# Performance work log

Hardware: AMD Instinct MI355X
Metric: run time of the kernel (lower is better)

The kernel has to match this reference:

```python
import jax, jax.numpy as jnp
import numpy as np

B, H, T, K, V, S = 2, 8, 4096, 128, 128, 128
C = T // S


def setup_inputs() -> dict:
    key = jax.random.key(0)
    ks = jax.random.split(key, 5)
    return {
        "q": jax.random.normal(ks[0], (B, H, T, K), jnp.float32),
        "k": jax.random.normal(ks[1], (B, H, T, K), jnp.float32),
        "v": jax.random.normal(ks[2], (B, H, T, V), jnp.float32),
        "i": jax.random.normal(ks[3], (B, H, T), jnp.float32),
        "f": jax.random.normal(ks[4], (B, H, T), jnp.float32),
        "initial_C": jnp.zeros((B, H, K, V), jnp.float32),
        "initial_n": jnp.zeros((B, H, K), jnp.float32),
        "initial_m": jnp.zeros((B, H), jnp.float32),
    }


def _forward(q, k, v, ig, fg, C0, n0, m0):
    scale = 1.0 / np.sqrt(K)
    q = q.reshape(B, H, C, S, K) * scale
    k = k.reshape(B, H, C, S, K)
    v = v.reshape(B, H, C, S, V)
    i = ig.reshape(B, H, C, S)
    lf = jax.nn.log_sigmoid(fg).reshape(B, H, C, S)

    lfacc = jnp.cumsum(lf, axis=3)          # backward gates (intra-chunk cumsum)
    lflast = lfacc[..., -1]                  # (B,H,C) total log-forget per chunk
    # rev_cumsum_off: sum of log_fgates strictly after position t
    fwd_gates_unstab = i + (lflast[..., None] - lfacc)
    m_intra = jnp.max(fwd_gates_unstab, axis=3)          # (B,H,C)
    fgexp = jnp.exp(fwd_gates_unstab - m_intra[..., None])

    kv = jnp.einsum("bhctk,bhctd,bhct->bhckd", k, v, fgexp)
    ksum = jnp.einsum("bhctk,bhct->bhck", k, fgexp)

    # sequential inter-chunk recurrence over C chunks (stabilized)
    def step(carry, xs):
        c, n, m = carry
        kv_j, ks_j, lfl_j, mi_j = xs
        m_new = jnp.maximum(lfl_j + m, mi_j)
        e1 = jnp.exp(lfl_j + m - m_new)   # (B,H)
        e2 = jnp.exp(mi_j - m_new)
        out = (c, n, m)                    # state BEFORE this chunk
        c = c * e1[..., None, None] + kv_j * e2[..., None, None]
        n = n * e1[..., None] + ks_j * e2[..., None]
        return (c, n, m), out

    xs = (jnp.moveaxis(kv, 2, 0), jnp.moveaxis(ksum, 2, 0),
          jnp.moveaxis(lflast, 2, 0), jnp.moveaxis(m_intra, 2, 0))
    _, (c_prev, n_prev, m_prev) = jax.lax.scan(step, (C0, n0, m0), xs)
    c_prev = jnp.moveaxis(c_prev, 0, 2)   # (B,H,C,K,V)
    n_prev = jnp.moveaxis(n_prev, 0, 2)   # (B,H,C,K)
    m_prev = jnp.moveaxis(m_prev, 0, 2)   # (B,H,C)

    # intra-chunk causal forget matrix: G_unstab[s,t] = sum_{u=t+1..s} lf[u] + i[t]
    D = lfacc[..., :, None] - lfacc[..., None, :]        # (B,H,C,S,S)
    mask = jnp.tril(jnp.ones((S, S), bool))
    G_unstab = jnp.where(mask, D + i[:, :, :, None, :], -jnp.inf)
    G_stab = jnp.max(G_unstab, axis=-1)                   # (B,H,C,S)
    G_stab = jnp.maximum(G_stab, m_prev[..., None] + lfacc)
    G = jnp.exp(G_unstab - G_stab[..., None])             # -inf -> 0

    M = jnp.einsum("bhctk,bhcsk,bhcst->bhcst", k, q, G)
    inter_w = jnp.exp(lfacc + m_prev[..., None] - G_stab)  # (B,H,C,S)
    inter_n = jnp.einsum("bhcsk,bhcs,bhck->bhcs", q, inter_w, n_prev)
    M_norm = jnp.maximum(jnp.abs(M.sum(-1) + inter_n), jnp.exp(-G_stab))

    h = jnp.einsum("bhctv,bhcst,bhcs->bhcsv", v, M, 1.0 / M_norm)
    h = h + jnp.einsum("bhckv,bhcsk,bhcs->bhcsv", c_prev, q, inter_w / M_norm)
    return h.reshape(B, H, T, V)


def reference(q, k, v, i, f, initial_C, initial_n, initial_m):
    return _forward(q, k, v, i, f, initial_C, initial_n, initial_m)
```

## Files before the change

### kernel.cpp

```cpp
#include <hip/hip_runtime.h>
#include <hip/hip_fp16.h>
#include <math.h>

#define Bb 2
#define Hh 8
#define Tt 4096
#define Kk 128
#define Vv 128
#define Ss 128
#define Cc 32
#define BH (Bb*Hh)
#define SCALE 0.08838834764831845f

#define OFF_LFACC  0
#define OFF_LFLAST (OFF_LFACC + BH*Tt)
#define OFF_MINTRA (OFF_LFLAST + BH*Cc)
#define OFF_KSUM   (OFF_MINTRA + BH*Cc)
#define OFF_KVH    (OFF_KSUM + BH*Cc*Kk)
#define OFF_KIMG   (OFF_KVH + BH*Cc*Kk*Vv/2)
#define OFF_VIMG   (OFF_KIMG + BH*Tt*Kk/2)

typedef _Float16 f16x8 __attribute__((ext_vector_type(8)));
typedef _Float16 f16x4 __attribute__((ext_vector_type(4)));
typedef _Float16 f16x2 __attribute__((ext_vector_type(2)));
typedef float f32x4 __attribute__((ext_vector_type(4)));

union U2 { f16x2 h; unsigned u; };
union U8 { f16x8 v; unsigned u[4]; };

#define GLDS16(gp, lp) __builtin_amdgcn_global_load_lds( \
    (const __attribute__((address_space(1))) void*)(gp), \
    (__attribute__((address_space(3))) void*)(lp), 16, 0, 0)

__global__ __launch_bounds__(512, 4) void k_kvg(const float* __restrict__ ig,
                                                const float* __restrict__ fg,
                                                const float* __restrict__ kg,
                                                const float* __restrict__ vg,
                                                float* __restrict__ ws) {
    __shared__ _Float16 Kt[Ss * Ss];
    __shared__ _Float16 Vt[Ss * Ss];
    __shared__ float sfg[Ss];
    __shared__ float scomb[4];

    int blk = blockIdx.x;
    int bh = blk >> 5;
    int c  = blk & 31;
    int tid = threadIdx.x;
    int lane = tid & 63;
    int w = tid >> 6;
    int l15 = lane & 15;
    int g = lane >> 4;

    const float* kb = kg + ((size_t)bh * Tt + (size_t)c * Ss) * Kk;
    const float* vb = vg + ((size_t)bh * Tt + (size_t)c * Ss) * Vv;
    _Float16* kimgw = (_Float16*)(ws + OFF_KIMG) + (size_t)blk * Ss * Kk;
    _Float16* vimgw = (_Float16*)(ws + OFF_VIMG) + (size_t)blk * Ss * Kk;

    int c0a = (tid & 31) * 4;
    int t0a = (tid >> 5) * 4;
    const float* ksrcA = kb + (size_t)t0a * Kk + c0a;
    const float* vsrcA = vb + (size_t)t0a * Vv + c0a;
    float4 kA0 = *(const float4*)(ksrcA);
    float4 kA1 = *(const float4*)(ksrcA + Kk);
    float4 kA2 = *(const float4*)(ksrcA + 2 * Kk);
    float4 kA3 = *(const float4*)(ksrcA + 3 * Kk);
    float4 vA0 = *(const float4*)(vsrcA);
    float4 vA1 = *(const float4*)(vsrcA + Vv);
    float4 vA2 = *(const float4*)(vsrcA + 2 * Vv);
    float4 vA3 = *(const float4*)(vsrcA + 3 * Vv);
    int tau1 = tid + 512;
    int c0b = (tau1 & 31) * 4;
    int t0b = (tau1 >> 5) * 4;
    const float* ksrcB = kb + (size_t)t0b * Kk + c0b;
    const float* vsrcB = vb + (size_t)t0b * Vv + c0b;
    float4 kB0 = *(const float4*)(ksrcB);
    float4 kB1 = *(const float4*)(ksrcB + Kk);
    float4 kB2 = *(const float4*)(ksrcB + 2 * Kk);
    float4 kB3 = *(const float4*)(ksrcB + 3 * Kk);
    float4 vB0 = *(const float4*)(vsrcB);
    float4 vB1 = *(const float4*)(vsrcB + Vv);
    float4 vB2 = *(const float4*)(vsrcB + 2 * Vv);
    float4 vB3 = *(const float4*)(vsrcB + 3 * Vv);

    bool p0 = tid < Ss;
    int lane64 = tid & 63;
    int wv = (tid >> 6) & 1;
    int gidx = bh * Tt + c * Ss + tid;
    float lfacc = 0.f, fwd = 0.f;
    if (p0) {
        float x  = fg[gidx];
        lfacc = fminf(x, 0.f) - log1pf(__expf(-fabsf(x)));
        for (int off = 1; off < 64; off <<= 1) {
            float o = __shfl_up(lfacc, off);
            if (lane64 >= off) lfacc += o;
        }
        if (lane64 == 63) scomb[wv] = lfacc;
    }
    __syncthreads();
    if (p0) {
        float tot0 = scomb[0];
        if (wv == 1) lfacc += tot0;
        float lflast = tot0 + scomb[1];
        fwd = ig[gidx] + lflast - lfacc;
        float mx = fwd;
        for (int off = 32; off; off >>= 1) mx = fmaxf(mx, __shfl_xor(mx, off));
        if (lane64 == 0) scomb[2 + wv] = mx;
    }
    __syncthreads();
    if (p0) {
        float mi = fmaxf(scomb[2], scomb[3]);
        sfg[tid] = __expf(fwd - mi);
        ws[OFF_LFACC + gidx] = lfacc;
        if (tid == 0) {
            ws[OFF_LFLAST + blk] = scomb[0] + scomb[1];
            ws[OFF_MINTRA + blk] = mi;
        }
    }
    __syncthreads();

#pragma unroll
    for (int jr = 0; jr < 4; jr++) {
        float4 kr4 = (jr == 0 ? kA0 : jr == 1 ? kA1 : jr == 2 ? kA2 : kA3);
        int t = t0a + jr;
        int col = c0a ^ ((t & 15) << 3);
        f16x4 h = { (_Float16)kr4.x, (_Float16)kr4.y, (_Float16)kr4.z, (_Float16)kr4.w };
        *(f16x4*)&kimgw[(size_t)t * Kk + col] = h;
    }
#pragma unroll
    for (int jr = 0; jr < 4; jr++) {
        float4 kr4 = (jr == 0 ? kB0 : jr == 1 ? kB1 : jr == 2 ? kB2 : kB3);
        int t = t0b + jr;
        int col = c0b ^ ((t & 15) << 3);
        f16x4 h = { (_Float16)kr4.x, (_Float16)kr4.y, (_Float16)kr4.z, (_Float16)kr4.w };
        *(f16x4*)&kimgw[(size_t)t * Kk + col] = h;
    }

    {
        float g0 = sfg[t0a], g1 = sfg[t0a + 1], g2 = sfg[t0a + 2], g3 = sfg[t0a + 3];
#pragma unroll
        for (int jc = 0; jc < 4; jc++) {
            float ke0 = (jc == 0 ? kA0.x : jc == 1 ? kA0.y : jc == 2 ? kA0.z : kA0.w);
            float ke1 = (jc == 0 ? kA1.x : jc == 1 ? kA1.y : jc == 2 ? kA1.z : kA1.w);
            float ke2 = (jc == 0 ? kA2.x : jc == 1 ? kA2.y : jc == 2 ? kA2.z : kA2.w);
            float ke3 = (jc == 0 ? kA3.x : jc == 1 ? kA3.y : jc == 2 ? kA3.z : kA3.w);
            float ve0 = (jc == 0 ? vA0.x : jc == 1 ? vA0.y : jc == 2 ? vA0.z : vA0.w);
            float ve1 = (jc == 0 ? vA1.x : jc == 1 ? vA1.y : jc == 2 ? vA1.z : vA1.w);
            float ve2 = (jc == 0 ? vA2.x : jc == 1 ? vA2.y : jc == 2 ? vA2.z : vA2.w);
            float ve3 = (jc == 0 ? vA3.x : jc == 1 ? vA3.y : jc == 2 ? vA3.z : vA3.w);
            int row = c0a + jc;
            int col = t0a ^ ((row & 15) << 3);
            f16x4 kc = { (_Float16)(ke0 * g0), (_Float16)(ke1 * g1),
                         (_Float16)(ke2 * g2), (_Float16)(ke3 * g3) };
            f16x4 vc = { (_Float16)ve0, (_Float16)ve1, (_Float16)ve2, (_Float16)ve3 };
            *(f16x4*)&Kt[row * Ss + col] = kc;
            *(f16x4*)&Vt[row * Ss + col] = vc;
        }
    }
    {
        float g0 = sfg[t0b], g1 = sfg[t0b + 1], g2 = sfg[t0b + 2], g3 = sfg[t0b + 3];
#pragma unroll
        for (int jc = 0; jc < 4; jc++) {
            float ke0 = (jc == 0 ? kB0.x : jc == 1 ? kB0.y : jc == 2 ? kB0.z : kB0.w);
            float ke1 = (jc == 0 ? kB1.x : jc == 1 ? kB1.y : jc == 2 ? kB1.z : kB1.w);
            float ke2 = (jc == 0 ? kB2.x : jc == 1 ? kB2.y : jc == 2 ? kB2.z : kB2.w);
            float ke3 = (jc == 0 ? kB3.x : jc == 1 ? kB3.y : jc == 2 ? kB3.z : kB3.w);
            float ve0 = (jc == 0 ? vB0.x : jc == 1 ? vB0.y : jc == 2 ? vB0.z : vB0.w);
            float ve1 = (jc == 0 ? vB1.x : jc == 1 ? vB1.y : jc == 2 ? vB1.z : vB1.w);
            float ve2 = (jc == 0 ? vB2.x : jc == 1 ? vB2.y : jc == 2 ? vB2.z : vB2.w);
            float ve3 = (jc == 0 ? vB3.x : jc == 1 ? vB3.y : jc == 2 ? vB3.z : vB3.w);
            int row = c0b + jc;
            int col = t0b ^ ((row & 15) << 3);
            f16x4 kc = { (_Float16)(ke0 * g0), (_Float16)(ke1 * g1),
                         (_Float16)(ke2 * g2), (_Float16)(ke3 * g3) };
            f16x4 vc = { (_Float16)ve0, (_Float16)ve1, (_Float16)ve2, (_Float16)ve3 };
            *(f16x4*)&Kt[row * Ss + col] = kc;
            *(f16x4*)&Vt[row * Ss + col] = vc;
        }
    }
    __syncthreads();

#pragma unroll
    for (int p = 0; p < 4; p++)
        *(f16x8*)&vimgw[(size_t)(p * 512 + tid) * 8] =
            *(const f16x8*)&Vt[(p * 512 + tid) * 8];

    if (tid < Ss) {
        int sw = (tid & 15) << 3;
        float s = 0.f;
#pragma unroll
        for (int i = 0; i < 16; i++) {
            f16x8 ld = *(const f16x8*)&Kt[tid * Ss + ((8 * i) ^ sw)];
#pragma unroll
            for (int e = 0; e < 8; e++) s += (float)ld[e];
        }
        ws[OFF_KSUM + (size_t)blk * Kk + tid] = s;
    }

    const int band = w * 16;
    const int swt = l15 << 3;
    f16x8 af[4];
#pragma unroll
    for (int kk = 0; kk < 4; kk++)
        af[kk] = *(const f16x8*)&Vt[(band + l15) * Ss + ((kk * 32 + g * 8) ^ swt)];

    f32x4 acc[8];
#pragma unroll
    for (int kj = 0; kj < 8; kj++) acc[kj] = (f32x4){0.f, 0.f, 0.f, 0.f};

#pragma unroll
    for (int kj = 0; kj < 8; kj++) {
        int kr = kj * 16 + l15;
#pragma unroll
        for (int kk = 0; kk < 4; kk++) {
            f16x8 bv = *(const f16x8*)&Kt[kr * Ss + ((kk * 32 + g * 8) ^ swt)];
            acc[kj] = __builtin_amdgcn_mfma_f32_16x16x32_f16(af[kk], bv, acc[kj], 0, 0, 0);
        }
    }

    _Float16* dst = (_Float16*)(ws + OFF_KVH) + (size_t)blk * Kk * Vv;
#pragma unroll
    for (int kj = 0; kj < 8; kj++)
#pragma unroll
        for (int r = 0; r < 4; r++)
            dst[(size_t)(band + 4 * g + r) * Kk + kj * 16 + l15] = (_Float16)acc[kj][r];
}

__global__ __launch_bounds__(128) void k_scan_apply(const float* __restrict__ C0,
                                                    const float* __restrict__ n0,
                                                    const float* __restrict__ m0,
                                                    float* __restrict__ ws) {
    __shared__ float se1[Cc], se2[Cc];
    const int NC2 = BH * Kk * Vv / 2;
    int gid = blockIdx.x * 128 + threadIdx.x;
    bool main_r = gid < NC2;
    int bh = main_r ? (gid >> 13) : ((gid - NC2) >> 7);

    if (threadIdx.x < Cc) {
        int cc = threadIdx.x;
        float m   = m0[bh];
        float lfl = ws[OFF_LFLAST + bh * Cc + cc];
        float mi  = ws[OFF_MINTRA + bh * Cc + cc];
        float mn  = fmaxf(lfl + m, mi);
        se1[cc] = __expf(lfl + m - mn);
        se2[cc] = __expf(mi - mn);
    }
    __syncthreads();

    if (main_r) {
        int i  = gid & 8191;
        int v  = i >> 6;
        int k2 = (i & 63) << 1;
        float st0 = C0[(size_t)bh * Kk * Vv + (size_t)k2 * Vv + v];
        float st1 = C0[(size_t)bh * Kk * Vv + (size_t)(k2 + 1) * Vv + v];
        f16x2* base = (f16x2*)((_Float16*)(ws + OFF_KVH) +
                               (size_t)bh * Cc * Kk * Vv + (size_t)v * Kk + k2);
        const size_t stride = Kk * Vv / 2;
        f16x2 cur = base[0];
        f16x2 nxt = base[stride];
#pragma unroll
        for (int c = 0; c < Cc; c++) {
            f16x2 n2 = (c + 2 < Cc) ? base[(size_t)(c + 2) * stride]
                                    : (f16x2){(_Float16)0.f, (_Float16)0.f};
            f16x2 o = { (_Float16)st0, (_Float16)st1 };
            base[(size_t)c * stride] = o;
            float e1 = se1[c], e2 = se2[c];
            st0 = st0 * e1 + (float)cur[0] * e2;
            st1 = st1 * e1 + (float)cur[1] * e2;
            cur = nxt; nxt = n2;
        }
    } else if (gid < NC2 + BH * Kk) {
        int g2 = gid - NC2;
        float st = n0[g2];
        float* base = ws + OFF_KSUM + (size_t)bh * Cc * Kk + (g2 & (Kk - 1));
        float cur = base[0];
        float nxt = base[Kk];
#pragma unroll
        for (int c = 0; c < Cc; c++) {
            float n2 = (c + 2 < Cc) ? base[(size_t)(c + 2) * Kk] : 0.f;
            float kvv = cur;
            base[(size_t)c * Kk] = st;
            st = st * se1[c] + kvv * se2[c];
            cur = nxt; nxt = n2;
        }
    }
}

__global__ __launch_bounds__(512, 4) void k_out_mfma(const float* __restrict__ qg,
                                                     const float* __restrict__ ig,
                                                     const float* __restrict__ m0,
                                                     float* __restrict__ ws,
                                                     float* __restrict__ out) {
    __shared__ _Float16 XbK[Ss * Kk];
    __shared__ _Float16 XbV[Ss * Kk];
    __shared__ float sbt[Ss], sas[Ss], siw[Ss], slfa[Ss], snp[Ss];
    __shared__ float scomb[2];

    int blk = blockIdx.x;
    int bh = blk >> 5;
    int c  = blk & 31;
    int tid = threadIdx.x;
    int lane = tid & 63;
    int w = tid >> 6;
    int l15 = lane & 15;
    int g = lane >> 4;
    const int S0 = w * 16;
    const int swt = l15 << 3;

    const size_t rowbase = (size_t)bh * Tt + (size_t)c * Ss;
    const float* qp = qg + rowbase * Kk;
    const float* nprev = ws + OFF_KSUM + (size_t)blk * Kk;
    const _Float16* cprevT = (const _Float16*)(ws + OFF_KVH) + (size_t)blk * Kk * Vv;
    const _Float16* kimg = (const _Float16*)(ws + OFF_KIMG) + (size_t)blk * Ss * Kk;
    const _Float16* vimg = (const _Float16*)(ws + OFF_VIMG) + (size_t)blk * Ss * Kk;
    const float m_prev = m0[bh];

#pragma unroll
    for (int p = 0; p < 4; p++) {
        int unit = p * 512 + w * 64;
        GLDS16(kimg + (size_t)(unit + lane) * 8, &XbK[unit * 8]);
        GLDS16(vimg + (size_t)(unit + lane) * 8, &XbV[unit * 8]);
    }

    f16x8 qf[4];
#pragma unroll
    for (int kk = 0; kk < 4; kk++) {
        const float* p = qp + (size_t)(S0 + l15) * Kk + kk * 32 + g * 8;
        float4 a = *(const float4*)p;
        float4 b = *(const float4*)(p + 4);
        f16x8 r;
        r[0]=(_Float16)a.x; r[1]=(_Float16)a.y; r[2]=(_Float16)a.z; r[3]=(_Float16)a.w;
        r[4]=(_Float16)b.x; r[5]=(_Float16)b.y; r[6]=(_Float16)b.z; r[7]=(_Float16)b.w;
        qf[kk] = r;
    }

    bool p0 = tid < Ss;
    int lane64 = tid & 63;
    int wv = (tid >> 6) & 1;
    float pm = 0.f;
    if (p0) {
        float lfa = ws[OFF_LFACC + bh * Tt + c * Ss + tid];
        float bt = ig[bh * Tt + c * Ss + tid] - lfa;
        sbt[tid] = bt;
        slfa[tid] = lfa;
        snp[tid] = nprev[tid];
        pm = bt;
        for (int off = 1; off < 64; off <<= 1) {
            float o = __shfl_up(pm, off);
            if (lane64 >= off) pm = fmaxf(pm, o);
        }
        if (lane64 == 63) scomb[wv] = pm;
    }
    __syncthreads();

    if (p0) {
        if (wv == 1) pm = fmaxf(pm, scomb[0]);
        float mx = fmaxf(pm, m_prev);
        sas[tid] = -mx;
        siw[tid] = SCALE * __expf(m_prev - mx);
    }
    float dotq = 0.f;
#pragma unroll
    for (int kk = 0; kk < 4; kk++)
#pragma unroll
        for (int e = 0; e < 8; e++)
            dotq += (float)qf[kk][e] * snp[kk * 32 + g * 8 + e];
    dotq += __shfl_xor(dotq, 16);
    dotq += __shfl_xor(dotq, 32);
    __syncthreads();

    const float as_s = sas[S0 + l15];
    const float iw_s = siw[S0 + l15];
    const float lfa_s = slfa[S0 + l15];

    unsigned plo[8] = {0,0,0,0,0,0,0,0};
    unsigned phi[8] = {0,0,0,0,0,0,0,0};
    float rs = 0.f;
#pragma unroll
    for (int tj = 0; tj < 8; tj++) {
        if (tj <= w) {
            int trow = tj * 16 + l15;
            f16x8 bfr[4];
#pragma unroll
            for (int kk = 0; kk < 4; kk++)
                bfr[kk] = *(const f16x8*)&XbK[trow * Kk + ((kk * 32 + g * 8) ^ swt)];
            f32x4 acc = {0.f, 0.f, 0.f, 0.f};
#pragma unroll
            for (int kk = 0; kk < 4; kk++)
                acc = __builtin_amdgcn_mfma_f32_16x16x32_f16(bfr[kk], qf[kk], acc, 0, 0, 0);
            float vals[4];
#pragma unroll
            for (int r = 0; r < 4; r++) {
                int t = tj * 16 + 4 * g + r;
                float btv = sbt[t];
                float val = acc[r] * SCALE * __expf(as_s + btv);
                if (tj == w && (4 * g + r) > l15) val = 0.f;
                rs += val;
                vals[r] = val;
            }
            U2 lo, hi;
            lo.h = (f16x2){ (_Float16)vals[0], (_Float16)vals[1] };
            hi.h = (f16x2){ (_Float16)vals[2], (_Float16)vals[3] };
            plo[tj] = lo.u;
            phi[tj] = hi.u;
        }
    }
    rs += __shfl_xor(rs, 16);
    rs += __shfl_xor(rs, 32);
    float engs = __expf(as_s - lfa_s);
    float rnv_s = 1.0f / fmaxf(fabsf(rs + dotq * iw_s), engs);

    f16x8 pb[4];
    const int kmax = w >> 1;
    {
        int a2 = (g & 1) * 2;
        int sA = a2 * 16 + l15;
        int sB = sA + 16;
        bool hi2 = (g >> 1) != 0;
#pragma unroll
        for (int kkt = 0; kkt < 4; kkt++) {
            if (kkt <= kmax) {
                unsigned xA0 = __shfl((int)plo[2*kkt],   sA);
                unsigned xA1 = __shfl((int)phi[2*kkt],   sA);
                unsigned xB0 = __shfl((int)plo[2*kkt],   sB);
                unsigned xB1 = __shfl((int)phi[2*kkt],   sB);
                unsigned yA0 = __shfl((int)plo[2*kkt+1], sA);
                unsigned yA1 = __shfl((int)phi[2*kkt+1], sA);
                unsigned yB0 = __shfl((int)plo[2*kkt+1], sB);
                unsigned yB1 = __shfl((int)phi[2*kkt+1], sB);
                U8 t;
                t.u[0] = hi2 ? yA0 : xA0;
                t.u[1] = hi2 ? yA1 : xA1;
                t.u[2] = hi2 ? yB0 : xB0;
                t.u[3] = hi2 ? yB1 : xB1;
                pb[kkt] = t.v;
            }
        }
    }

#pragma unroll
    for (int half = 0; half < 2; half++) {
        f32x4 h4[4];
#pragma unroll
        for (int j = 0; j < 4; j++) h4[j] = (f32x4){0.f, 0.f, 0.f, 0.f};

#pragma unroll
        for (int kkt = 0; kkt < 4; kkt++) {
            if (kkt <= kmax) {
#pragma unroll
                for (int j = 0; j < 4; j++) {
                    int vr = (half * 4 + j) * 16 + l15;
                    f16x8 av = *(const f16x8*)&XbV[vr * Ss + ((kkt * 32 + g * 8) ^ swt)];
                    h4[j] = __builtin_amdgcn_mfma_f32_16x16x32_f16(av, pb[kkt], h4[j], 0, 0, 0);
                }
            }
        }
#pragma unroll
        for (int j = 0; j < 4; j++) {
            int vr = (half * 4 + j) * 16 + l15;
            f32x4 tmp = {0.f, 0.f, 0.f, 0.f};
            const _Float16* cpr = cprevT + (size_t)vr * Kk + g * 8;
#pragma unroll
            for (int kk = 0; kk < 4; kk++) {
                f16x8 bcf = *(const f16x8*)(cpr + kk * 32);
                tmp = __builtin_amdgcn_mfma_f32_16x16x32_f16(bcf, qf[kk], tmp, 0, 0, 0);
            }
            float4 o;
            o.x = (h4[j][0] + tmp[0] * iw_s) * rnv_s;
            o.y = (h4[j][1] + tmp[1] * iw_s) * rnv_s;
            o.z = (h4[j][2] + tmp[2] * iw_s) * rnv_s;
            o.w = (h4[j][3] + tmp[3] * iw_s) * rnv_s;
            *(float4*)&out[(rowbase + S0 + l15) * Vv + (half * 4 + j) * 16 + 4 * g] = o;
        }
    }
}

extern "C" void kernel_launch(void* const* d_in, const int* in_sizes, int n_in,
                              void* d_out, int out_size, void* d_ws, size_t ws_size,
                              hipStream_t stream) {
    (void)in_sizes; (void)n_in; (void)out_size; (void)ws_size;
    const float* q  = (const float*)d_in[0];
    const float* k  = (const float*)d_in[1];
    const float* v  = (const float*)d_in[2];
    const float* ig = (const float*)d_in[3];
    const float* fg = (const float*)d_in[4];
    const float* C0 = (const float*)d_in[5];
    const float* n0 = (const float*)d_in[6];
    const float* m0 = (const float*)d_in[7];
    float* out = (float*)d_out;
    float* ws  = (float*)d_ws;

    k_kvg<<<BH * Cc, 512, 0, stream>>>(ig, fg, k, v, ws);
    k_scan_apply<<<(BH * Kk * Vv / 2 + BH * Kk) / 128, 128, 0, stream>>>(C0, n0, m0, ws);
    k_out_mfma<<<BH * Cc, 512, 0, stream>>>(q, ig, m0, ws, out);
}
```

Before: 60.67 us.

## Stage swizzled C_prev tile into LDS asynchronously and reorder K-image writes

The output kernel used to read the per-chunk C_prev state straight from global memory inside the MFMA loop. It now issues direct global-to-LDS loads into the reused K buffer after a barrier, overlaps them with the intra-chunk PV MFMAs, and then reads C_prev from LDS. To keep those LDS reads free of bank conflicts, the kv writer and the scan kernel store C_prev with an XOR-swizzled column layout. The f16 K-image stores are also moved ahead of the gate scan so they overlap with the log-sigmoid and cumsum work. In exchange the change adds barriers and keeps more accumulators live (h4 doubled), which raises register pressure.

```diff
diff --git a/kernel.cpp b/kernel.cpp
--- a/kernel.cpp
+++ b/kernel.cpp
@@ -82,6 +82,23 @@
     float4 vB2 = *(const float4*)(vsrcB + 2 * Vv);
     float4 vB3 = *(const float4*)(vsrcB + 3 * Vv);
 
+#pragma unroll
+    for (int jr = 0; jr < 4; jr++) {
+        float4 kr4 = (jr == 0 ? kA0 : jr == 1 ? kA1 : jr == 2 ? kA2 : kA3);
+        int t = t0a + jr;
+        int col = c0a ^ ((t & 15) << 3);
+        f16x4 h = { (_Float16)kr4.x, (_Float16)kr4.y, (_Float16)kr4.z, (_Float16)kr4.w };
+        *(f16x4*)&kimgw[(size_t)t * Kk + col] = h;
+    }
+#pragma unroll
+    for (int jr = 0; jr < 4; jr++) {
+        float4 kr4 = (jr == 0 ? kB0 : jr == 1 ? kB1 : jr == 2 ? kB2 : kB3);
+        int t = t0b + jr;
+        int col = c0b ^ ((t & 15) << 3);
+        f16x4 h = { (_Float16)kr4.x, (_Float16)kr4.y, (_Float16)kr4.z, (_Float16)kr4.w };
+        *(f16x4*)&kimgw[(size_t)t * Kk + col] = h;
+    }
+
     bool p0 = tid < Ss;
     int lane64 = tid & 63;
     int wv = (tid >> 6) & 1;
@@ -117,23 +134,6 @@
         }
     }
     __syncthreads();
-
-#pragma unroll
-    for (int jr = 0; jr < 4; jr++) {
-        float4 kr4 = (jr == 0 ? kA0 : jr == 1 ? kA1 : jr == 2 ? kA2 : kA3);
-        int t = t0a + jr;
-        int col = c0a ^ ((t & 15) << 3);
-        f16x4 h = { (_Float16)kr4.x, (_Float16)kr4.y, (_Float16)kr4.z, (_Float16)kr4.w };
-        *(f16x4*)&kimgw[(size_t)t * Kk + col] = h;
-    }
-#pragma unroll
-    for (int jr = 0; jr < 4; jr++) {
-        float4 kr4 = (jr == 0 ? kB0 : jr == 1 ? kB1 : jr == 2 ? kB2 : kB3);
-        int t = t0b + jr;
-        int col = c0b ^ ((t & 15) << 3);
-        f16x4 h = { (_Float16)kr4.x, (_Float16)kr4.y, (_Float16)kr4.z, (_Float16)kr4.w };
-        *(f16x4*)&kimgw[(size_t)t * Kk + col] = h;
-    }
 
     {
         float g0 = sfg[t0a], g1 = sfg[t0a + 1], g2 = sfg[t0a + 2], g3 = sfg[t0a + 3];
@@ -221,8 +221,11 @@
 #pragma unroll
     for (int kj = 0; kj < 8; kj++)
 #pragma unroll
-        for (int r = 0; r < 4; r++)
-            dst[(size_t)(band + 4 * g + r) * Kk + kj * 16 + l15] = (_Float16)acc[kj][r];
+        for (int r = 0; r < 4; r++) {
+            int vrow = band + 4 * g + r;
+            int col = (kj * 16 + l15) ^ ((vrow & 15) << 3);
+            dst[(size_t)vrow * Kk + col] = (_Float16)acc[kj][r];
+        }
 }
 
 __global__ __launch_bounds__(128) void k_scan_apply(const float* __restrict__ C0,
@@ -249,11 +252,12 @@
     if (main_r) {
         int i  = gid & 8191;
         int v  = i >> 6;
-        int k2 = (i & 63) << 1;
-        float st0 = C0[(size_t)bh * Kk * Vv + (size_t)k2 * Vv + v];
-        float st1 = C0[(size_t)bh * Kk * Vv + (size_t)(k2 + 1) * Vv + v];
+        int j2 = (i & 63) << 1;
+        int klog = j2 ^ ((v & 15) << 3);
+        float st0 = C0[(size_t)bh * Kk * Vv + (size_t)klog * Vv + v];
+        float st1 = C0[(size_t)bh * Kk * Vv + (size_t)(klog + 1) * Vv + v];
         f16x2* base = (f16x2*)((_Float16*)(ws + OFF_KVH) +
-                               (size_t)bh * Cc * Kk * Vv + (size_t)v * Kk + k2);
+                               (size_t)bh * Cc * Kk * Vv + (size_t)v * Kk + j2);
         const size_t stride = Kk * Vv / 2;
         f16x2 cur = base[0];
         f16x2 nxt = base[stride];
@@ -408,6 +412,13 @@
     rs += __shfl_xor(rs, 32);
     float engs = __expf(as_s - lfa_s);
     float rnv_s = 1.0f / fmaxf(fabsf(rs + dotq * iw_s), engs);
+    __syncthreads();
+
+#pragma unroll
+    for (int p = 0; p < 4; p++) {
+        int u = w * 4 + p;
+        GLDS16(cprevT + (size_t)(u * 64 + lane) * 8, &XbK[u * 512]);
+    }
 
     f16x8 pb[4];
     const int kmax = w >> 1;
@@ -437,41 +448,48 @@
         }
     }
 
-#pragma unroll
-    for (int half = 0; half < 2; half++) {
-        f32x4 h4[4];
-#pragma unroll
-        for (int j = 0; j < 4; j++) h4[j] = (f32x4){0.f, 0.f, 0.f, 0.f};
-
-#pragma unroll
-        for (int kkt = 0; kkt < 4; kkt++) {
-            if (kkt <= kmax) {
+    f32x4 h4[2][4];
+#pragma unroll
+    for (int half = 0; half < 2; half++)
+#pragma unroll
+        for (int j = 0; j < 4; j++) h4[half][j] = (f32x4){0.f, 0.f, 0.f, 0.f};
+
+#pragma unroll
+    for (int kkt = 0; kkt < 4; kkt++) {
+        if (kkt <= kmax) {
+#pragma unroll
+            for (int half = 0; half < 2; half++)
 #pragma unroll
                 for (int j = 0; j < 4; j++) {
                     int vr = (half * 4 + j) * 16 + l15;
                     f16x8 av = *(const f16x8*)&XbV[vr * Ss + ((kkt * 32 + g * 8) ^ swt)];
-                    h4[j] = __builtin_amdgcn_mfma_f32_16x16x32_f16(av, pb[kkt], h4[j], 0, 0, 0);
+                    h4[half][j] = __builtin_amdgcn_mfma_f32_16x16x32_f16(av, pb[kkt], h4[half][j], 0, 0, 0);
                 }
-            }
-        }
+        }
+    }
+
+    asm volatile("s_waitcnt vmcnt(0)" ::: "memory");
+    __syncthreads();
+
+#pragma unroll
+    for (int half = 0; half < 2; half++)
 #pragma unroll
         for (int j = 0; j < 4; j++) {
             int vr = (half * 4 + j) * 16 + l15;
             f32x4 tmp = {0.f, 0.f, 0.f, 0.f};
-            const _Float16* cpr = cprevT + (size_t)vr * Kk + g * 8;
+            int swv = (vr & 15) << 3;
 #pragma unroll
             for (int kk = 0; kk < 4; kk++) {
-                f16x8 bcf = *(const f16x8*)(cpr + kk * 32);
+                f16x8 bcf = *(const f16x8*)&XbK[vr * Kk + ((kk * 32 + g * 8) ^ swv)];
                 tmp = __builtin_amdgcn_mfma_f32_16x16x32_f16(bcf, qf[kk], tmp, 0, 0, 0);
             }
             float4 o;
-            o.x = (h4[j][0] + tmp[0] * iw_s) * rnv_s;
-            o.y = (h4[j][1] + tmp[1] * iw_s) * rnv_s;
-            o.z = (h4[j][2] + tmp[2] * iw_s) * rnv_s;
-            o.w = (h4[j][3] + tmp[3] * iw_s) * rnv_s;
+            o.x = (h4[half][j][0] + tmp[0] * iw_s) * rnv_s;
+            o.y = (h4[half][j][1] + tmp[1] * iw_s) * rnv_s;
+            o.z = (h4[half][j][2] + tmp[2] * iw_s) * rnv_s;
+            o.w = (h4[half][j][3] + tmp[3] * iw_s) * rnv_s;
             *(float4*)&out[(rowbase + S0 + l15) * Vv + (half * 4 + j) * 16 + 4 * g] = o;
         }
-    }
 }
 
 extern "C" void kernel_launch(void* const* d_in, const int* in_sizes, int n_in,
```

Result: faster. 53.08 us (-12.5%).
